# Kernel optimization log

Measured on AMD Instinct MI355X. Metric: run time of the kernel, lower is better.

Reference implementation:

```python
import jax, jax.numpy as jnp
import numpy as np
import math

R, C, B, E, H, F = 64, 256, 1, 768, 12, 3072
D = E // H  # head dim = 64
EPS = 1e-6  # flax LayerNorm default


def _ln(x, s, b):
    mu = jnp.mean(x, axis=-1, keepdims=True)
    var = jnp.mean((x - mu) ** 2, axis=-1, keepdims=True)
    return (x - mu) * jax.lax.rsqrt(var + EPS) * s + b


def setup_inputs() -> dict:
    key = jax.random.key(0)
    ks = jax.random.split(key, 16)
    w = lambda k, sh: jax.random.normal(k, sh, jnp.float32) * 0.02
    z = lambda sh: jnp.zeros(sh, jnp.float32)
    return {
        "x": jax.random.normal(ks[0], (R, C, B, E), jnp.float32),
        "ln1_s": jnp.ones((E,), jnp.float32), "ln1_b": z((E,)),
        "r_wq": w(ks[1], (E, E)), "r_bq": z((E,)),
        "r_wk": w(ks[2], (E, E)), "r_bk": z((E,)),
        "r_wv": w(ks[3], (E, E)), "r_bv": z((E,)),
        "r_wo": w(ks[4], (E, E)), "r_bo": z((E,)),
        "ln2_s": jnp.ones((E,), jnp.float32), "ln2_b": z((E,)),
        "c_wq": w(ks[5], (E, E)), "c_bq": z((E,)),
        "c_wk": w(ks[6], (E, E)), "c_bk": z((E,)),
        "c_wv": w(ks[7], (E, E)), "c_bv": z((E,)),
        "c_wo": w(ks[8], (E, E)), "c_bo": z((E,)),
        "ln3_s": jnp.ones((E,), jnp.float32), "ln3_b": z((E,)),
        "f_w1": w(ks[9], (E, F)), "f_b1": z((F,)),
        "f_w2": w(ks[10], (F, E)), "f_b2": z((E,)),
    }


def reference(x, ln1_s, ln1_b, r_wq, r_bq, r_wk, r_bk, r_wv, r_bv, r_wo, r_bo,
              ln2_s, ln2_b, c_wq, c_bq, c_wk, c_bk, c_wv, c_bv, c_wo, c_bo,
              ln3_s, ln3_b, f_w1, f_b1, f_w2, f_b2):
    qkv = (R, C, B, H, D)
    # --- tied row self-attention (NOTE: original code has no residual adds) ---
    h = _ln(x, ln1_s, ln1_b)
    q = (h @ r_wq + r_bq).reshape(qkv) * (D ** -0.5 / math.sqrt(R))  # tied-row scaling
    k = (h @ r_wk + r_bk).reshape(qkv)
    v = (h @ r_wv + r_bv).reshape(qkv)
    aw = jnp.einsum('rinhd,rjnhd->hnij', q, k)  # single softmax tied across rows
    ap = jax.nn.softmax(aw, axis=-1)
    ctx = jnp.einsum('hnij,rjnhd->rinhd', ap, v).reshape(R, C, B, E)
    x = ctx @ r_wo + r_bo
    # --- column self-attention (per-column attention over rows) ---
    h = _ln(x, ln2_s, ln2_b)
    q = (h @ c_wq + c_bq).reshape(qkv) * (D ** -0.5)
    k = (h @ c_wk + c_bk).reshape(qkv)
    v = (h @ c_wv + c_bv).reshape(qkv)
    aw = jnp.einsum('icnhd,jcnhd->hcnij', q, k)
    ap = jax.nn.softmax(aw, axis=-1)
    ctx = jnp.einsum('hcnij,jcnhd->icnhd', ap, v).reshape(R, C, B, E)
    x = ctx @ c_wo + c_bo
    # --- FFN (gelu approximate=True matches flax default) ---
    h = _ln(x, ln3_s, ln3_b)
    return jax.nn.gelu(h @ f_w1 + f_b1) @ f_w2 + f_b2
```

## Files before the change

kernel.cpp:

```cpp
#include <hip/hip_runtime.h>
#include <hip/hip_bf16.h>
#include <stdint.h>
#include <stddef.h>

#define R_ 64
#define C_ 256
#define E_ 768
#define H_ 12
#define F_ 3072
#define D_ 64
#define NT_ (R_*C_)
#define HCRD_ ((size_t)H_*C_*R_*D_)

typedef float f32x4 __attribute__((ext_vector_type(4)));
typedef __bf16 bf16x8 __attribute__((ext_vector_type(8)));
typedef unsigned short us4 __attribute__((ext_vector_type(4)));
typedef unsigned short us8 __attribute__((ext_vector_type(8)));

typedef __attribute__((address_space(3))) uint32_t lds_u32;
typedef __attribute__((address_space(1))) uint32_t glb_u32;

__device__ __forceinline__ void gld16(const uint16_t* g, uint16_t* l) {
  __builtin_amdgcn_global_load_lds((const glb_u32*)g, (lds_u32*)l, 16, 0, 0);
}

__device__ __forceinline__ uint16_t f2b(float f) {
  __bf16 h = (__bf16)f;
  return *(uint16_t*)&h;
}

#define TILE_SYNC { asm volatile("s_waitcnt vmcnt(0)" ::: "memory"); \
                    __builtin_amdgcn_s_barrier(); \
                    __builtin_amdgcn_sched_barrier(0); }
#define BAR_ONLY  { __builtin_amdgcn_s_barrier(); __builtin_amdgcn_sched_barrier(0); }

enum { EP_F32B = 0, EP_GELU = 1, EP_AW = 2, EP_CTX = 3, EP_QKVROW = 4, EP_QKVCOL = 5 };

template<int EP, bool PERM>
__global__ __launch_bounds__(512, 2)
void gemm256(const uint16_t* __restrict__ A, const uint16_t* __restrict__ B,
             const float* __restrict__ bias, const float* __restrict__ biasK,
             const float* __restrict__ biasV, void* __restrict__ out,
             int N, int K, int lda, int ldb, float scale)
{
  __shared__ uint16_t As2[2][16384];
  __shared__ uint16_t Bs2[2][16384];
  const int tid  = threadIdx.x;
  const int wave = tid >> 6, lane = tid & 63;
  const int wm = wave >> 2, wn = wave & 3;
  const int lr = lane & 15, lq = lane >> 4;

  int lin = blockIdx.x + gridDim.x * blockIdx.y;
  const int q8 = (gridDim.x * gridDim.y) >> 3;
  const int wid = (lin & 7) * q8 + (lin >> 3);
  const int bx = wid % gridDim.x, by = wid / gridDim.x;
  const long bm = (long)by * 256, bn = (long)bx * 256;

  const int r0 = tid >> 3;
  const int c8 = (((tid & 7) ^ (r0 & 7)) << 3);
  const uint16_t* aSrc[4];
  const uint16_t* bSrc[4];
#pragma unroll
  for (int i = 0; i < 4; ++i) {
    long am = bm + r0 + 64 * i;
    if constexpr (PERM) am = ((am & 63) << 8) | (am >> 6);
    aSrc[i] = A + am * (long)lda + c8;
    bSrc[i] = B + (bn + r0 + 64 * i) * (long)ldb + c8;
  }

  auto stage = [&](int u) {
    const int b = u & 1;
    const int kb = u << 6;
#pragma unroll
    for (int i = 0; i < 4; ++i) gld16(aSrc[i] + kb, &As2[b][tid * 8 + 4096 * i]);
#pragma unroll
    for (int i = 0; i < 4; ++i) gld16(bSrc[i] + kb, &Bs2[b][tid * 8 + 4096 * i]);
  };
  auto rdoff = [&](int row, int c) { return row * 64 + (((c ^ (row & 7))) << 3); };

  f32x4 acc[8][4];
#pragma unroll
  for (int i = 0; i < 8; ++i)
#pragma unroll
    for (int j = 0; j < 4; ++j) acc[i][j] = (f32x4){0.f, 0.f, 0.f, 0.f};

  const int nt = K >> 6;
  stage(0);
  TILE_SYNC;

  for (int t = 0; t < nt; ++t) {
    const int b = t & 1;
    if (t + 1 < nt) stage(t + 1);
#pragma unroll
    for (int kh = 0; kh < 2; ++kh) {
      const int c = kh * 4 + lq;
      bf16x8 bfr[4], afr[8];
#pragma unroll
      for (int i = 0; i < 4; ++i) bfr[i] = *(const bf16x8*)&Bs2[b][rdoff(wn * 64 + i * 16 + lr, c)];
#pragma unroll
      for (int i = 0; i < 8; ++i) afr[i] = *(const bf16x8*)&As2[b][rdoff(wm * 128 + i * 16 + lr, c)];
      __builtin_amdgcn_s_setprio(1);
#pragma unroll
      for (int mi = 0; mi < 8; ++mi)
#pragma unroll
        for (int ni = 0; ni < 4; ++ni)
          acc[mi][ni] = __builtin_amdgcn_mfma_f32_16x16x32_bf16(afr[mi], bfr[ni], acc[mi][ni], 0, 0, 0);
      __builtin_amdgcn_s_setprio(0);
    }
    if (t + 1 < nt) { TILE_SYNC; } else { BAR_ONLY; }
  }
  __syncthreads();

  if constexpr (EP == EP_F32B) {
#pragma unroll
    for (int mi = 0; mi < 8; ++mi)
#pragma unroll
      for (int ni = 0; ni < 4; ++ni)
#pragma unroll
        for (int r = 0; r < 4; ++r) {
          const long row = bm + wm * 128 + mi * 16 + lq * 4 + r;
          const long col = bn + wn * 64 + ni * 16 + lr;
          ((float*)out)[row * N + col] = acc[mi][ni][r] + bias[col];
        }
  } else {
    uint16_t* slabW = (wave < 4) ? &As2[0][wave * 8192] : &Bs2[0][(wave - 4) * 8192];
    const long colb = bn + wn * 64;
    int grp = 0; long cc0 = colb;
    const float* bb = bias;
    if constexpr (EP != EP_GELU) {
      grp = colb >= 1536 ? 2 : (colb >= 768 ? 1 : 0);
      cc0 = colb - (long)grp * 768;
      bb = grp == 0 ? bias : (grp == 1 ? biasK : biasV);
    }
    const bool tr = (EP != EP_GELU) && (grp == 2);
#pragma unroll
    for (int sub = 0; sub < 2; ++sub) {
      uint16_t* slab = slabW + sub * 4096;
      const long m0 = bm + wm * 128 + sub * 64;
#pragma unroll
      for (int mi = 0; mi < 4; ++mi)
#pragma unroll
        for (int ni = 0; ni < 4; ++ni)
#pragma unroll
          for (int r = 0; r < 4; ++r) {
            const int lrow = mi * 16 + lq * 4 + r;
            const int lcol = ni * 16 + lr;
            float val;
            if constexpr (EP == EP_GELU) {
              const float t = acc[sub * 4 + mi][ni][r] + bias[colb + lcol];
              const float u = 0.7978845608028654f * (t + 0.044715f * t * t * t);
              const float e = __expf(2.f * u);
              val = 0.5f * t * (2.f - 2.f / (e + 1.f));
            } else {
              val = acc[sub * 4 + mi][ni][r] + bb[cc0 + lcol];
              if (grp == 0) val *= scale;
            }
            const int sr = tr ? lcol : lrow;
            const int sc = tr ? lrow : lcol;
            const int psc = (sc & 7) | ((((sc >> 3) ^ (sr & 7))) << 3);
            slab[sr * 64 + psc] = f2b(val);
          }
      uint16_t* o16 = (uint16_t*)out;
      long obase, rstride;
      if constexpr (EP == EP_GELU) {
        obase = m0 * (long)N + colb; rstride = N;
      } else {
        const long h = cc0 >> 6;
        if constexpr (EP == EP_QKVROW) {
          const long rr = m0 >> 8, c0 = m0 & 255;
          if (grp < 2) { obase = (size_t)grp * HCRD_ + ((h * C_ + c0) * R_ + rr) * D_; rstride = R_ * D_; }
          else         { obase = 2 * HCRD_ + ((h * R_ + rr) * D_) * C_ + c0;           rstride = C_; }
        } else {
          const long cq = m0 >> 6;
          if (grp < 2) { obase = (size_t)grp * HCRD_ + ((h * C_ + cq) * R_) * D_; rstride = D_; }
          else         { obase = 2 * HCRD_ + ((h * C_ + cq) * D_) * R_;           rstride = R_; }
        }
      }
      const int rl = lane >> 3, chn = lane & 7;
#pragma unroll
      for (int pp = 0; pp < 8; ++pp) {
        const int srow = pp * 8 + rl;
        const int pch = chn ^ (srow & 7);
        us8 wv = *(const us8*)&slab[srow * 64 + pch * 8];
        *(us8*)(o16 + obase + (long)srow * rstride + chn * 8) = wv;
      }
    }
  }
}

template<int EP>
__global__ __launch_bounds__(256)
void gemm_bt(const uint16_t* __restrict__ A, const uint16_t* __restrict__ B,
             void* __restrict__ out,
             int M, int N, int K, int lda, int ldb, long sAz, long sBz)
{
  __shared__ uint16_t As[2][4096];
  __shared__ uint16_t Bs[2][4096];
  const int tid  = threadIdx.x;
  const int wave = tid >> 6, lane = tid & 63;
  const int z = blockIdx.z;

  const long bm = (long)blockIdx.y * 128;
  int kc = 0; long bnb = blockIdx.x;
  if constexpr (EP == EP_AW) { kc = blockIdx.x & 3; bnb = blockIdx.x >> 2; }
  const long bn = bnb * 128;
  const int wr = (wave >> 1) * 64;
  const int wc = (wave & 1) * 64;
  const int lr = lane & 15;
  const int lq = lane >> 4;

  const int t0 = tid, t1 = tid + 256;
  const int ar0 = t0 >> 2, ar1 = t1 >> 2;
  const int ac0 = (((t0 & 3) ^ ((ar0 >> 1) & 3)) * 8);
  const int ac1 = (((t1 & 3) ^ ((ar1 >> 1) & 3)) * 8);

  const uint16_t* a0p = A + (long)z * sAz + (bm + ar0) * (long)lda + (long)kc * 1024;
  const uint16_t* a1p = A + (long)z * sAz + (bm + ar1) * (long)lda + (long)kc * 1024;
  const uint16_t* b0p = B + (long)z * sBz + (bn + ar0) * (long)ldb + (long)kc * 1024;
  const uint16_t* b1p = B + (long)z * sBz + (bn + ar1) * (long)ldb + (long)kc * 1024;

  auto STAGE = [&](int bi, int kt) {
    gld16(a0p + kt + ac0, &As[bi][t0 * 8]);
    gld16(a1p + kt + ac1, &As[bi][t1 * 8]);
    gld16(b0p + kt + ac0, &Bs[bi][t0 * 8]);
    gld16(b1p + kt + ac1, &Bs[bi][t1 * 8]);
  };

  int apos[4], bpos[4];
#pragma unroll
  for (int i = 0; i < 4; ++i) {
    const int ra = wr + i * 16 + lr;
    const int rb = wc + i * 16 + lr;
    apos[i] = ra * 32 + (lq ^ ((ra >> 1) & 3)) * 8;
    bpos[i] = rb * 32 + (lq ^ ((rb >> 1) & 3)) * 8;
  }

  f32x4 acc[4][4];
#pragma unroll
  for (int i = 0; i < 4; ++i)
#pragma unroll
    for (int j = 0; j < 4; ++j) acc[i][j] = (f32x4){0.f, 0.f, 0.f, 0.f};

  const int nt = K >> 5;
  STAGE(0, 0);
  TILE_SYNC;

  for (int t = 0; t < nt; ++t) {
    const int b = t & 1;
    if (t + 1 < nt) STAGE(b ^ 1, (t + 1) << 5);
    bf16x8 af[4], bfm[4];
#pragma unroll
    for (int i = 0; i < 4; ++i) {
      af[i]  = *(const bf16x8*)&As[b][apos[i]];
      bfm[i] = *(const bf16x8*)&Bs[b][bpos[i]];
    }
    __builtin_amdgcn_s_setprio(1);
#pragma unroll
    for (int mi = 0; mi < 4; ++mi)
#pragma unroll
      for (int ni = 0; ni < 4; ++ni)
        acc[mi][ni] = __builtin_amdgcn_mfma_f32_16x16x32_bf16(af[mi], bfm[ni], acc[mi][ni], 0, 0, 0);
    __builtin_amdgcn_s_setprio(0);
    if (t + 1 < nt) { TILE_SYNC; }
  }

#pragma unroll
  for (int mi = 0; mi < 4; ++mi)
#pragma unroll
    for (int ni = 0; ni < 4; ++ni)
#pragma unroll
      for (int r = 0; r < 4; ++r) {
        const long row = bm + wr + mi * 16 + lq * 4 + r;
        const long col = bn + wc + ni * 16 + lr;
        if constexpr (EP == EP_AW) {
          ((float*)out)[((long)(z * 4 + kc) * M + row) * N + col] = acc[mi][ni][r];
        } else {
          ((uint16_t*)out)[((col >> 6) * C_ + row) * E_ + (long)z * 64 + (col & 63)] =
              f2b(acc[mi][ni][r]);
        }
      }
}

__global__ __launch_bounds__(256)
void ln_k(const float* __restrict__ x, const float* __restrict__ s, const float* __restrict__ b,
          uint16_t* __restrict__ out)
{
  const int wave = threadIdx.x >> 6, lane = threadIdx.x & 63;
  const long row = (long)blockIdx.x * 4 + wave;
  const float* xr = x + row * E_;
  f32x4 v[3];
  float sum = 0.f, sq = 0.f;
#pragma unroll
  for (int i = 0; i < 3; ++i) {
    v[i] = *(const f32x4*)(xr + (i * 64 + lane) * 4);
#pragma unroll
    for (int j = 0; j < 4; ++j) { sum += v[i][j]; sq += v[i][j] * v[i][j]; }
  }
#pragma unroll
  for (int m = 1; m < 64; m <<= 1) { sum += __shfl_xor(sum, m); sq += __shfl_xor(sq, m); }
  const float mu = sum * (1.f / E_);
  const float var = sq * (1.f / E_) - mu * mu;
  const float rs = rsqrtf(var + 1e-6f);
  uint16_t* orow = out + row * E_;
#pragma unroll
  for (int i = 0; i < 3; ++i) {
    const int e0 = (i * 64 + lane) * 4;
    us4 o;
#pragma unroll
    for (int j = 0; j < 4; ++j) o[j] = f2b((v[i][j] - mu) * rs * s[e0 + j] + b[e0 + j]);
    *(us4*)(orow + e0) = o;
  }
}

__global__ __launch_bounds__(256)
void softmax_k4(const float* __restrict__ aw4, uint16_t* __restrict__ ap)
{
  const int wave = threadIdx.x >> 6, lane = threadIdx.x & 63;
  const long row = (long)blockIdx.x * 4 + wave;
  const long h = row >> 8, i = row & 255;
  f32x4 v = (f32x4){0.f, 0.f, 0.f, 0.f};
#pragma unroll
  for (int kc = 0; kc < 4; ++kc) {
    f32x4 t = *(const f32x4*)(aw4 + (((h * 4 + kc) * C_ + i) * C_) + lane * 4);
#pragma unroll
    for (int j = 0; j < 4; ++j) v[j] += t[j];
  }
  float m = fmaxf(fmaxf(v[0], v[1]), fmaxf(v[2], v[3]));
#pragma unroll
  for (int k = 1; k < 64; k <<= 1) m = fmaxf(m, __shfl_xor(m, k));
  f32x4 e; float s = 0.f;
#pragma unroll
  for (int j = 0; j < 4; ++j) { e[j] = __expf(v[j] - m); s += e[j]; }
#pragma unroll
  for (int k = 1; k < 64; k <<= 1) s += __shfl_xor(s, k);
  const float inv = 1.f / s;
  us4 o;
#pragma unroll
  for (int j = 0; j < 4; ++j) o[j] = f2b(e[j] * inv);
  *(us4*)(ap + row * C_ + lane * 4) = o;
}

__global__ __launch_bounds__(256)
void tcvt(const float* __restrict__ in, uint16_t* __restrict__ out, int K, int N)
{
  __shared__ float t[32][33];
  const int tx = threadIdx.x, ty = threadIdx.y;
  const long k0 = (long)blockIdx.y * 32, n0 = (long)blockIdx.x * 32;
  for (int i = ty; i < 32; i += 8) t[i][tx] = in[(k0 + i) * N + n0 + tx];
  __syncthreads();
  for (int i = ty; i < 32; i += 8) out[(n0 + i) * K + k0 + tx] = f2b(t[tx][i]);
}

__global__ __launch_bounds__(64)
void colattn(const uint16_t* __restrict__ q, const uint16_t* __restrict__ k,
             const uint16_t* __restrict__ v, uint16_t* __restrict__ ctx)
{
  __shared__ uint16_t Qs[64 * 64];
  __shared__ uint16_t Ks[64 * 64];
  __shared__ uint16_t Vs[64 * 64];
  const int hc = blockIdx.x;
  const int h = hc >> 8, c = hc & 255;
  const int lane = threadIdx.x;
  const uint16_t* qb = q + (long)hc * (R_ * D_);
  const uint16_t* kb = k + (long)hc * (R_ * D_);
  const uint16_t* vb = v + (long)hc * (D_ * R_);
#pragma unroll
  for (int it = 0; it < 8; ++it) {
    const int o = (it * 64 + lane) * 8;
    gld16(qb + o, &Qs[o]);
    gld16(kb + o, &Ks[o]);
    gld16(vb + o, &Vs[o]);
  }
  asm volatile("s_waitcnt vmcnt(0)" ::: "memory");
  __builtin_amdgcn_sched_barrier(0);

  const int lr = lane & 15, lq = lane >> 4;
  f32x4 acc[4][4];
#pragma unroll
  for (int i = 0; i < 4; ++i)
#pragma unroll
    for (int j = 0; j < 4; ++j) acc[i][j] = (f32x4){0.f, 0.f, 0.f, 0.f};

#pragma unroll
  for (int kt = 0; kt < 2; ++kt) {
    bf16x8 af[4], bfm[4];
#pragma unroll
    for (int i = 0; i < 4; ++i) {
      af[i]  = *(const bf16x8*)&Qs[(i * 16 + lr) * 64 + kt * 32 + lq * 8];
      bfm[i] = *(const bf16x8*)&Ks[(i * 16 + lr) * 64 + kt * 32 + lq * 8];
    }
#pragma unroll
    for (int mi = 0; mi < 4; ++mi)
#pragma unroll
      for (int ni = 0; ni < 4; ++ni)
        acc[mi][ni] = __builtin_amdgcn_mfma_f32_16x16x32_bf16(af[mi], bfm[ni], acc[mi][ni], 0, 0, 0);
  }

#pragma unroll
  for (int mi = 0; mi < 4; ++mi) {
#pragma unroll
    for (int r = 0; r < 4; ++r) {
      float mx = fmaxf(fmaxf(acc[mi][0][r], acc[mi][1][r]), fmaxf(acc[mi][2][r], acc[mi][3][r]));
#pragma unroll
      for (int s = 1; s < 16; s <<= 1) mx = fmaxf(mx, __shfl_xor(mx, s));
      float e0 = __expf(acc[mi][0][r] - mx), e1 = __expf(acc[mi][1][r] - mx);
      float e2 = __expf(acc[mi][2][r] - mx), e3 = __expf(acc[mi][3][r] - mx);
      float sum = e0 + e1 + e2 + e3;
#pragma unroll
      for (int s = 1; s < 16; s <<= 1) sum += __shfl_xor(sum, s);
      const float inv = 1.f / sum;
      const int i = mi * 16 + lq * 4 + r;
      Qs[i * 64 +  0 + lr] = f2b(e0 * inv);
      Qs[i * 64 + 16 + lr] = f2b(e1 * inv);
      Qs[i * 64 + 32 + lr] = f2b(e2 * inv);
      Qs[i * 64 + 48 + lr] = f2b(e3 * inv);
    }
  }
  __syncthreads();

  f32x4 o_[4][4];
#pragma unroll
  for (int i = 0; i < 4; ++i)
#pragma unroll
    for (int j = 0; j < 4; ++j) o_[i][j] = (f32x4){0.f, 0.f, 0.f, 0.f};

#pragma unroll
  for (int kt = 0; kt < 2; ++kt) {
    bf16x8 pa[4], vv[4];
#pragma unroll
    for (int i = 0; i < 4; ++i) {
      pa[i] = *(const bf16x8*)&Qs[(i * 16 + lr) * 64 + kt * 32 + lq * 8];
      vv[i] = *(const bf16x8*)&Vs[(i * 16 + lr) * 64 + kt * 32 + lq * 8];
    }
#pragma unroll
    for (int mi = 0; mi < 4; ++mi)
#pragma unroll
      for (int ni = 0; ni < 4; ++ni)
        o_[mi][ni] = __builtin_amdgcn_mfma_f32_16x16x32_bf16(pa[mi], vv[ni], o_[mi][ni], 0, 0, 0);
  }

#pragma unroll
  for (int mi = 0; mi < 4; ++mi)
#pragma unroll
    for (int ni = 0; ni < 4; ++ni)
#pragma unroll
      for (int r = 0; r < 4; ++r) {
        const int i = mi * 16 + lq * 4 + r;
        const int d = ni * 16 + lr;
        ctx[((long)i * C_ + c) * E_ + h * 64 + d] = f2b(o_[mi][ni][r]);
      }
}

extern "C" void kernel_launch(void* const* d_in, const int* in_sizes, int n_in,
                              void* d_out, int out_size, void* d_ws, size_t ws_size,
                              hipStream_t stream)
{
  (void)in_sizes; (void)n_in; (void)out_size; (void)ws_size;
  const float* x     = (const float*)d_in[0];
  const float* ln1_s = (const float*)d_in[1];
  const float* ln1_b = (const float*)d_in[2];
  const float* r_wq  = (const float*)d_in[3];
  const float* r_bq  = (const float*)d_in[4];
  const float* r_wk  = (const float*)d_in[5];
  const float* r_bk  = (const float*)d_in[6];
  const float* r_wv  = (const float*)d_in[7];
  const float* r_bv  = (const float*)d_in[8];
  const float* r_wo  = (const float*)d_in[9];
  const float* r_bo  = (const float*)d_in[10];
  const float* ln2_s = (const float*)d_in[11];
  const float* ln2_b = (const float*)d_in[12];
  const float* c_wq  = (const float*)d_in[13];
  const float* c_bq  = (const float*)d_in[14];
  const float* c_wk  = (const float*)d_in[15];
  const float* c_bk  = (const float*)d_in[16];
  const float* c_wv  = (const float*)d_in[17];
  const float* c_bv  = (const float*)d_in[18];
  const float* c_wo  = (const float*)d_in[19];
  const float* c_bo  = (const float*)d_in[20];
  const float* ln3_s = (const float*)d_in[21];
  const float* ln3_b = (const float*)d_in[22];
  const float* f_w1  = (const float*)d_in[23];
  const float* f_b1  = (const float*)d_in[24];
  const float* f_w2  = (const float*)d_in[25];
  const float* f_b2  = (const float*)d_in[26];

  uint8_t* p = (uint8_t*)d_ws;
  auto take = [&p](size_t n) { uint8_t* r = p; p += (n + 255) & ~(size_t)255; return r; };

  uint16_t* wqkv1 = (uint16_t*)take((size_t)3 * E_ * E_ * 2);
  uint16_t* wqkv2 = (uint16_t*)take((size_t)3 * E_ * E_ * 2);
  uint16_t* rwoT  = (uint16_t*)take((size_t)E_ * E_ * 2);
  uint16_t* cwoT  = (uint16_t*)take((size_t)E_ * E_ * 2);
  uint16_t* w1T   = (uint16_t*)take((size_t)E_ * F_ * 2);
  uint16_t* w2T   = (uint16_t*)take((size_t)F_ * E_ * 2);
  uint16_t* hb    = (uint16_t*)take((size_t)NT_ * E_ * 2);
  uint16_t* qkvT  = (uint16_t*)take(3 * HCRD_ * 2);
  uint16_t* qT = qkvT, *kT = qkvT + HCRD_, *vT = qkvT + 2 * HCRD_;
  uint16_t* ctxb  = (uint16_t*)take((size_t)NT_ * E_ * 2);
  uint16_t* apb   = (uint16_t*)take((size_t)H_ * C_ * C_ * 2);
  uint16_t* g     = qkvT;
  float*    awb4  = (float*)ctxb;
  float*    x1    = (float*)d_out;

  const dim3 tb32(32, 8);
  const dim3 gEE(E_ / 32, E_ / 32);
  tcvt<<<gEE, tb32, 0, stream>>>(r_wq, wqkv1 + 0 * E_ * E_, E_, E_);
  tcvt<<<gEE, tb32, 0, stream>>>(r_wk, wqkv1 + 1 * E_ * E_, E_, E_);
  tcvt<<<gEE, tb32, 0, stream>>>(r_wv, wqkv1 + 2 * E_ * E_, E_, E_);
  tcvt<<<gEE, tb32, 0, stream>>>(c_wq, wqkv2 + 0 * E_ * E_, E_, E_);
  tcvt<<<gEE, tb32, 0, stream>>>(c_wk, wqkv2 + 1 * E_ * E_, E_, E_);
  tcvt<<<gEE, tb32, 0, stream>>>(c_wv, wqkv2 + 2 * E_ * E_, E_, E_);
  tcvt<<<gEE, tb32, 0, stream>>>(r_wo, rwoT, E_, E_);
  tcvt<<<gEE, tb32, 0, stream>>>(c_wo, cwoT, E_, E_);
  tcvt<<<dim3(F_ / 32, E_ / 32), tb32, 0, stream>>>(f_w1, w1T, E_, F_);
  tcvt<<<dim3(E_ / 32, F_ / 32), tb32, 0, stream>>>(f_w2, w2T, F_, E_);

  ln_k<<<NT_ / 4, 256, 0, stream>>>(x, ln1_s, ln1_b, hb);
  gemm256<EP_QKVROW, false><<<dim3(9, 64), 512, 0, stream>>>(
      hb, wqkv1, r_bq, r_bk, r_bv, qkvT, 3 * E_, E_, E_, E_, 0.015625f);
  gemm_bt<EP_AW><<<dim3(8, 2, H_), 256, 0, stream>>>(
      qT, kT, awb4, C_, C_, 1024, R_ * D_, R_ * D_, (long)C_ * R_ * D_, (long)C_ * R_ * D_);
  softmax_k4<<<(H_ * C_) / 4, 256, 0, stream>>>(awb4, apb);
  gemm_bt<EP_CTX><<<dim3((R_ * D_) / 128, 2, H_), 256, 0, stream>>>(
      apb, vT, ctxb, C_, R_ * D_, C_, C_, C_, (long)C_ * C_, (long)R_ * D_ * C_);
  gemm256<EP_F32B, false><<<dim3(3, 64), 512, 0, stream>>>(
      ctxb, rwoT, r_bo, nullptr, nullptr, x1, E_, E_, E_, E_, 1.f);

  ln_k<<<NT_ / 4, 256, 0, stream>>>(x1, ln2_s, ln2_b, hb);
  gemm256<EP_QKVCOL, true><<<dim3(9, 64), 512, 0, stream>>>(
      hb, wqkv2, c_bq, c_bk, c_bv, qkvT, 3 * E_, E_, E_, E_, 0.125f);
  colattn<<<H_ * C_, 64, 0, stream>>>(qT, kT, vT, ctxb);
  gemm256<EP_F32B, false><<<dim3(3, 64), 512, 0, stream>>>(
      ctxb, cwoT, c_bo, nullptr, nullptr, x1, E_, E_, E_, E_, 1.f);

  ln_k<<<NT_ / 4, 256, 0, stream>>>(x1, ln3_s, ln3_b, hb);
  gemm256<EP_GELU, false><<<dim3(12, 64), 512, 0, stream>>>(
      hb, w1T, f_b1, nullptr, nullptr, g, F_, E_, E_, E_, 1.f);
  gemm256<EP_F32B, false><<<dim3(3, 64), 512, 0, stream>>>(
      g, w2T, f_b2, nullptr, nullptr, d_out, E_, F_, F_, F_, 1.f);
}
```

Measured before the change: 596.6 us.

## Batch weight transposes into one launch, remap XCD tile order, drop setprio

Merges eight separate E×E weight transpose-convert launches into a single 3D-grid kernel that picks its source and destination from blockIdx.z, cutting launch overhead. It also changes the block-to-XCD mapping in gemm256 so each XCD gets a contiguous band of row tiles, meant to improve L2 reuse of the A operand. It removes the s_setprio raising around the MFMA loops in both GEMM kernels. The new mapping assumes gridDim.y is divisible by 8.

```diff
diff --git a/kernel.cpp b/kernel.cpp
--- a/kernel.cpp
+++ b/kernel.cpp
@@ -50,10 +50,11 @@
   const int wm = wave >> 2, wn = wave & 3;
   const int lr = lane & 15, lq = lane >> 4;
 
-  int lin = blockIdx.x + gridDim.x * blockIdx.y;
-  const int q8 = (gridDim.x * gridDim.y) >> 3;
-  const int wid = (lin & 7) * q8 + (lin >> 3);
-  const int bx = wid % gridDim.x, by = wid / gridDim.x;
+  const int lin = blockIdx.x + gridDim.x * blockIdx.y;
+  const int xcd = lin & 7, idx = lin >> 3;
+  const int nbyx = gridDim.y >> 3;
+  const int by = xcd * nbyx + idx / gridDim.x;
+  const int bx = idx % gridDim.x;
   const long bm = (long)by * 256, bn = (long)bx * 256;
 
   const int r0 = tid >> 3;
@@ -99,13 +100,11 @@
       for (int i = 0; i < 4; ++i) bfr[i] = *(const bf16x8*)&Bs2[b][rdoff(wn * 64 + i * 16 + lr, c)];
 #pragma unroll
       for (int i = 0; i < 8; ++i) afr[i] = *(const bf16x8*)&As2[b][rdoff(wm * 128 + i * 16 + lr, c)];
-      __builtin_amdgcn_s_setprio(1);
 #pragma unroll
       for (int mi = 0; mi < 8; ++mi)
 #pragma unroll
         for (int ni = 0; ni < 4; ++ni)
           acc[mi][ni] = __builtin_amdgcn_mfma_f32_16x16x32_bf16(afr[mi], bfr[ni], acc[mi][ni], 0, 0, 0);
-      __builtin_amdgcn_s_setprio(0);
     }
     if (t + 1 < nt) { TILE_SYNC; } else { BAR_ONLY; }
   }
@@ -254,13 +253,11 @@
       af[i]  = *(const bf16x8*)&As[b][apos[i]];
       bfm[i] = *(const bf16x8*)&Bs[b][bpos[i]];
     }
-    __builtin_amdgcn_s_setprio(1);
 #pragma unroll
     for (int mi = 0; mi < 4; ++mi)
 #pragma unroll
       for (int ni = 0; ni < 4; ++ni)
         acc[mi][ni] = __builtin_amdgcn_mfma_f32_16x16x32_bf16(af[mi], bfm[ni], acc[mi][ni], 0, 0, 0);
-    __builtin_amdgcn_s_setprio(0);
     if (t + 1 < nt) { TILE_SYNC; }
   }
 
@@ -349,6 +346,31 @@
   for (int i = ty; i < 32; i += 8) t[i][tx] = in[(k0 + i) * N + n0 + tx];
   __syncthreads();
   for (int i = ty; i < 32; i += 8) out[(n0 + i) * K + k0 + tx] = f2b(t[tx][i]);
+}
+
+__global__ __launch_bounds__(256)
+void tcvt8(const float* a0, const float* a1, const float* a2, const float* a3,
+           const float* a4, const float* a5, const float* a6, const float* a7,
+           uint16_t* o0, uint16_t* o1, uint16_t* o2, uint16_t* o3,
+           uint16_t* o4, uint16_t* o5, uint16_t* o6, uint16_t* o7)
+{
+  __shared__ float t[32][33];
+  const float* in; uint16_t* out;
+  switch (blockIdx.z) {
+    case 0: in = a0; out = o0; break;
+    case 1: in = a1; out = o1; break;
+    case 2: in = a2; out = o2; break;
+    case 3: in = a3; out = o3; break;
+    case 4: in = a4; out = o4; break;
+    case 5: in = a5; out = o5; break;
+    case 6: in = a6; out = o6; break;
+    default: in = a7; out = o7; break;
+  }
+  const int tx = threadIdx.x, ty = threadIdx.y;
+  const long k0 = (long)blockIdx.y * 32, n0 = (long)blockIdx.x * 32;
+  for (int i = ty; i < 32; i += 8) t[i][tx] = in[(k0 + i) * E_ + n0 + tx];
+  __syncthreads();
+  for (int i = ty; i < 32; i += 8) out[(n0 + i) * E_ + k0 + tx] = f2b(t[tx][i]);
 }
 
 __global__ __launch_bounds__(64)
@@ -503,15 +525,11 @@
   float*    x1    = (float*)d_out;
 
   const dim3 tb32(32, 8);
-  const dim3 gEE(E_ / 32, E_ / 32);
-  tcvt<<<gEE, tb32, 0, stream>>>(r_wq, wqkv1 + 0 * E_ * E_, E_, E_);
-  tcvt<<<gEE, tb32, 0, stream>>>(r_wk, wqkv1 + 1 * E_ * E_, E_, E_);
-  tcvt<<<gEE, tb32, 0, stream>>>(r_wv, wqkv1 + 2 * E_ * E_, E_, E_);
-  tcvt<<<gEE, tb32, 0, stream>>>(c_wq, wqkv2 + 0 * E_ * E_, E_, E_);
-  tcvt<<<gEE, tb32, 0, stream>>>(c_wk, wqkv2 + 1 * E_ * E_, E_, E_);
-  tcvt<<<gEE, tb32, 0, stream>>>(c_wv, wqkv2 + 2 * E_ * E_, E_, E_);
-  tcvt<<<gEE, tb32, 0, stream>>>(r_wo, rwoT, E_, E_);
-  tcvt<<<gEE, tb32, 0, stream>>>(c_wo, cwoT, E_, E_);
+  tcvt8<<<dim3(E_ / 32, E_ / 32, 8), tb32, 0, stream>>>(
+      r_wq, r_wk, r_wv, c_wq, c_wk, c_wv, r_wo, c_wo,
+      wqkv1 + 0 * E_ * E_, wqkv1 + 1 * E_ * E_, wqkv1 + 2 * E_ * E_,
+      wqkv2 + 0 * E_ * E_, wqkv2 + 1 * E_ * E_, wqkv2 + 2 * E_ * E_,
+      rwoT, cwoT);
   tcvt<<<dim3(F_ / 32, E_ / 32), tb32, 0, stream>>>(f_w1, w1T, E_, F_);
   tcvt<<<dim3(E_ / 32, F_ / 32), tb32, 0, stream>>>(f_w2, w2T, F_, E_);
 
```

Result: no change. 585.7 us (-1.8%).
